# Optimization experiments

Measured on AMD Instinct MI355X. Metric: run time of the kernel, lower is better.

Reference implementation:

```python
import jax, jax.numpy as jnp
import numpy as np

B, S, D = 1, 2048, 2048
H, G, HD = 32, 8, 64          # heads, kv groups, head_dim
GS = H // G                   # group size = 4
EPS = 1e-6


def _rmsnorm(v, w):
    vf = v.astype(jnp.float32)
    n = vf * jax.lax.rsqrt(jnp.mean(vf * vf, axis=-1, keepdims=True) + EPS)
    return (n * (1.0 + w.astype(jnp.float32))).astype(v.dtype)


def _rope(v, cos, sin):
    # v: [b, h, s, hd]; cos/sin: [s, hd] (rot_dim == head_dim)
    half = v.shape[-1] // 2
    x1, x2 = v[..., :half], v[..., half:]
    rotated = jnp.concatenate([-x2, x1], axis=-1)
    c = cos[None, None, :, :]
    s = sin[None, None, :, :]
    return (v * c + rotated * s).astype(v.dtype)


def setup_inputs() -> dict:
    key = jax.random.key(0)
    ks = jax.random.split(key, 8)
    x = jax.random.normal(ks[0], (B, S, D), dtype=jnp.float32)
    # causal mask: True above diagonal => masked out
    mask = jnp.triu(jnp.ones((S, S), dtype=bool), k=1)
    # standard RoPE tables, full rotary dim == head_dim
    inv_freq = 1.0 / (10000.0 ** (jnp.arange(0, HD, 2, dtype=jnp.float32) / HD))
    angles = jnp.arange(S, dtype=jnp.float32)[:, None] * inv_freq[None, :]
    angles = jnp.concatenate([angles, angles], axis=-1)  # [S, HD]
    cos = jnp.cos(angles)
    sin = jnp.sin(angles)
    sc = 1.0 / np.sqrt(D)
    Wq = jax.random.normal(ks[1], (2 * H * HD, D), dtype=jnp.float32) * sc
    Wk = jax.random.normal(ks[2], (G * HD, D), dtype=jnp.float32) * sc
    Wv = jax.random.normal(ks[3], (G * HD, D), dtype=jnp.float32) * sc
    Wo = jax.random.normal(ks[4], (D, H * HD), dtype=jnp.float32) * sc
    q_norm_w = jnp.zeros((HD,), dtype=jnp.float32)
    k_norm_w = jnp.zeros((HD,), dtype=jnp.float32)
    return {"x": x, "mask": mask, "cos": cos, "sin": sin, "Wq": Wq,
            "Wk": Wk, "Wv": Wv, "Wo": Wo,
            "q_norm_w": q_norm_w, "k_norm_w": k_norm_w}


def reference(x, mask, cos, sin, Wq, Wk, Wv, Wo, q_norm_w, k_norm_w):
    b, s, _ = x.shape
    d_out = H * HD
    # fused q + gate projection: [b, s, H, 2*HD]
    qg = jnp.einsum('bsd,ed->bse', x, Wq).reshape(b, s, H, 2 * HD)
    q = qg[..., :HD]                         # [b, s, H, HD]
    gate = qg[..., HD:].reshape(b, s, d_out)  # [b, s, d_out]
    k = jnp.einsum('bsd,ed->bse', x, Wk).reshape(b, s, G, HD)
    v = jnp.einsum('bsd,ed->bse', x, Wv).reshape(b, s, G, HD)
    q = q.transpose(0, 2, 1, 3)   # [b, H, s, HD]
    k = k.transpose(0, 2, 1, 3)   # [b, G, s, HD]
    v = v.transpose(0, 2, 1, 3)
    q = _rmsnorm(q, q_norm_w)
    k = _rmsnorm(k, k_norm_w)
    q = _rope(q, cos[:s], sin[:s])
    k = _rope(k, cos[:s], sin[:s])
    # GQA without materializing repeated K/V: group queries as [b, G, GS, s, HD]
    qg_ = q.reshape(b, G, GS, s, HD)
    scores = jnp.einsum('bghqd,bgkd->bghqk', qg_, k)   # [b, G, GS, s, s]
    scores = jnp.where(mask[None, None, None, :s, :s], -jnp.inf, scores)
    scale = HD ** (-0.5)
    w = jax.nn.softmax((scores * scale).astype(jnp.float32), axis=-1).astype(q.dtype)
    ctx = jnp.einsum('bghqk,bgkd->bghqd', w, v)        # [b, G, GS, s, HD]
    ctx = ctx.reshape(b, H, s, HD).transpose(0, 2, 1, 3).reshape(b, s, d_out)
    ctx = ctx * jax.nn.sigmoid(gate)
    return jnp.einsum('bse,de->bsd', ctx, Wo)
```

## Files before the change

### kernel.cpp

```cpp
#include <hip/hip_runtime.h>

typedef __bf16 bf16;
typedef __bf16 bf16x4 __attribute__((ext_vector_type(4)));
typedef __bf16 bf16x8 __attribute__((ext_vector_type(8)));
typedef float f32x4 __attribute__((ext_vector_type(4)));

#define DEV static __device__ __forceinline__

constexpr int S  = 2048;
constexpr int D  = 2048;
constexpr int H  = 32;
constexpr int G  = 8;
constexpr int HD = 64;
constexpr int NQG = 2 * H * HD;
constexpr int LDP = 136;

DEV bf16x8 load8(const bf16* p) { return *reinterpret_cast<const bf16x8*>(p); }

DEV f32x4 mfma16(bf16x8 a, bf16x8 b, f32x4 c) {
  return __builtin_amdgcn_mfma_f32_16x16x32_bf16(a, b, c, 0, 0, 0);
}

DEV void gload_lds16(const bf16* g, bf16* l) {
  __builtin_amdgcn_global_load_lds(
      (const __attribute__((address_space(1))) void*)g,
      (__attribute__((address_space(3))) void*)l, 16, 0, 0);
}

#define BARRIER() asm volatile("s_barrier" ::: "memory")
#define VMDRAIN() asm volatile("s_waitcnt vmcnt(0)" ::: "memory")

template <int NISS>
DEV void stage_tile(bf16* lds, const bf16* src_row0, size_t ld, int k0, int tid) {
  const int w = tid >> 6, l = tid & 63;
#pragma unroll
  for (int i = 0; i < NISS; ++i) {
    int blk = w * NISS + i;
    int r = blk * 8 + (l >> 3);
    int c = (l & 7) ^ (r & 7);
    gload_lds16(src_row0 + (size_t)r * ld + k0 + c * 8, lds + blk * 512);
  }
}

DEV void stage64_8w(bf16* lds, const bf16* src_row0, size_t ld, int k0, int tid) {
  const int w = tid >> 6, l = tid & 63;
  int r = w * 8 + (l >> 3);
  int c = (l & 7) ^ (r & 7);
  gload_lds16(src_row0 + (size_t)r * ld + k0 + c * 8, lds + w * 512);
}

DEV bf16x8 fragr(const bf16* T, int row, int chunk) {
  return load8(T + row * 64 + (((chunk ^ (row & 7)) << 3)));
}

DEV float fexp2(float x) { return __builtin_amdgcn_exp2f(x); }
DEV float frcp(float x)  { return __builtin_amdgcn_rcpf(x); }

__global__ __launch_bounds__(256) void cvt_all(
    const float* __restrict__ x,  const float* __restrict__ wq,
    const float* __restrict__ wk, const float* __restrict__ wv,
    bf16* __restrict__ xb,  bf16* __restrict__ wqb, bf16* __restrict__ wkb,
    bf16* __restrict__ wvb)
{
  long c = (long)blockIdx.x * 256 + threadIdx.x;
  const float* src; bf16* dst; long off;
  if      (c <  524288) { src = x;  dst = xb;  off = c; }
  else if (c < 1572864) { src = wq; dst = wqb; off = c -  524288; }
  else if (c < 1703936) { src = wk; dst = wkb; off = c - 1572864; }
  else                  { src = wv; dst = wvb; off = c - 1703936; }
  long i = off * 8;
  const float4* p = reinterpret_cast<const float4*>(src + i);
  float4 a = p[0], b = p[1];
  bf16x8 o;
  o[0] = (bf16)a.x; o[1] = (bf16)a.y; o[2] = (bf16)a.z; o[3] = (bf16)a.w;
  o[4] = (bf16)b.x; o[5] = (bf16)b.y; o[6] = (bf16)b.z; o[7] = (bf16)b.w;
  *reinterpret_cast<bf16x8*>(dst + i) = o;
}

DEV void rms_rope_store(f32x4 acc[4][4], bf16* __restrict__ dst,
                        const float* __restrict__ w,
                        const float* __restrict__ cosb,
                        const float* __restrict__ sinb,
                        int s0, int ln, int hi, float outscale)
{
  float wgt[4];
#pragma unroll
  for (int ni = 0; ni < 4; ++ni) wgt[ni] = 1.0f + w[ni * 16 + ln];
#pragma unroll
  for (int mi = 0; mi < 4; ++mi)
#pragma unroll
    for (int j = 0; j < 4; ++j) {
      int s = s0 + mi * 16 + hi * 4 + j;
      float v0 = acc[mi][0][j], v1 = acc[mi][1][j];
      float v2 = acc[mi][2][j], v3 = acc[mi][3][j];
      float ss = v0 * v0 + v1 * v1 + v2 * v2 + v3 * v3;
      ss += __shfl_xor(ss, 1);
      ss += __shfl_xor(ss, 2);
      ss += __shfl_xor(ss, 4);
      ss += __shfl_xor(ss, 8);
      float inv = __builtin_amdgcn_rsqf(ss * (1.0f / 64.0f) + 1e-6f);
      float xf[4] = {v0 * inv * wgt[0], v1 * inv * wgt[1],
                     v2 * inv * wgt[2], v3 * inv * wgt[3]};
#pragma unroll
      for (int ni = 0; ni < 4; ++ni) {
        int d = ni * 16 + ln;
        float c  = cosb[s * HD + d];
        float sn = sinb[s * HD + d];
        float rot = (ni < 2) ? -xf[ni + 2] : xf[ni - 2];
        dst[(size_t)s * HD + d] = (bf16)((xf[ni] * c + rot * sn) * outscale);
      }
    }
}

__global__ __launch_bounds__(256, 3) void gemm_qkv(
    const bf16* __restrict__ X, const bf16* __restrict__ Wq,
    const bf16* __restrict__ Wk, const bf16* __restrict__ Wv,
    const float* __restrict__ cosb, const float* __restrict__ sinb,
    const float* __restrict__ qw, const float* __restrict__ kw,
    const float* __restrict__ wo, bf16* __restrict__ wob,
    bf16* __restrict__ qg, bf16* __restrict__ qrot,
    bf16* __restrict__ krot, bf16* __restrict__ vt)
{
  __shared__ __align__(16) bf16 As[128 * 64];
  __shared__ __align__(16) bf16 Bs[128 * 64];

  const int tid  = threadIdx.x;
  const int nt = blockIdx.x;

  if (nt >= 40) {
    long base = (long)((nt - 40) * 16 + blockIdx.y) * 256 + tid;
#pragma unroll
    for (int it = 0; it < 16; ++it) {
      long i = (base + (long)it * 32768) * 8;
      const float4* p = reinterpret_cast<const float4*>(wo + i);
      float4 a = p[0], b = p[1];
      bf16x8 o;
      o[0] = (bf16)a.x; o[1] = (bf16)a.y; o[2] = (bf16)a.z; o[3] = (bf16)a.w;
      o[4] = (bf16)b.x; o[5] = (bf16)b.y; o[6] = (bf16)b.z; o[7] = (bf16)b.w;
      *reinterpret_cast<bf16x8*>(wob + i) = o;
    }
    return;
  }

  const int wave = tid >> 6;
  const int lane = tid & 63;
  const int ln = lane & 15, hi = lane >> 4;
  const int wm = wave >> 1, wn = wave & 1;
  const int m0 = blockIdx.y * 128;

  const bf16* W; int n0;
  if (nt < 32)      { W = Wq; n0 = nt * 128; }
  else if (nt < 36) { W = Wk; n0 = (nt - 32) * 128; }
  else              { W = Wv; n0 = (nt - 36) * 128; }

  const bf16* arow = X + (size_t)m0 * D;
  const bf16* brow = W + (size_t)n0 * D;

  f32x4 acc[4][4] = {};

  for (int k0 = 0; k0 < D; k0 += 64) {
    __syncthreads();
    stage_tile<4>(As, arow, D, k0, tid);
    stage_tile<4>(Bs, brow, D, k0, tid);
    __syncthreads();
#pragma unroll
    for (int kk = 0; kk < 64; kk += 32) {
      bf16x8 a[4], b[4];
#pragma unroll
      for (int mi = 0; mi < 4; ++mi) a[mi] = fragr(As, wm * 64 + mi * 16 + ln, (kk >> 3) + hi);
#pragma unroll
      for (int ni = 0; ni < 4; ++ni) b[ni] = fragr(Bs, wn * 64 + ni * 16 + ln, (kk >> 3) + hi);
#pragma unroll
      for (int mi = 0; mi < 4; ++mi)
#pragma unroll
        for (int ni = 0; ni < 4; ++ni)
          acc[mi][ni] = mfma16(a[mi], b[ni], acc[mi][ni]);
    }
  }

  const int s0 = m0 + wm * 64;
  if (nt < 32) {
    if (wn == 0) {
      rms_rope_store(acc, qrot + (size_t)nt * S * HD, qw, cosb, sinb,
                     s0, ln, hi, 0.18033688011111204f);
    } else {
#pragma unroll
      for (int mi = 0; mi < 4; ++mi)
#pragma unroll
        for (int ni = 0; ni < 4; ++ni)
#pragma unroll
          for (int j = 0; j < 4; ++j) {
            int r = s0 + mi * 16 + hi * 4 + j;
            int c = nt * 128 + 64 + ni * 16 + ln;
            qg[(size_t)r * NQG + c] = (bf16)acc[mi][ni][j];
          }
    }
  } else if (nt < 36) {
    int g8 = (nt - 32) * 2 + wn;
    rms_rope_store(acc, krot + (size_t)g8 * S * HD, kw, cosb, sinb,
                   s0, ln, hi, 1.0f);
  } else {
    int nrel = (nt - 36) * 128;
#pragma unroll
    for (int mi = 0; mi < 4; ++mi)
#pragma unroll
      for (int ni = 0; ni < 4; ++ni)
#pragma unroll
        for (int j = 0; j < 4; ++j) {
          int r = s0 + mi * 16 + hi * 4 + j;
          int c = nrel + wn * 64 + ni * 16 + ln;
          vt[(size_t)c * S + r] = (bf16)acc[mi][ni][j];
        }
  }
}

__global__ __launch_bounds__(256, 3) void gemm_out(
    const bf16* __restrict__ A, const bf16* __restrict__ W,
    float* __restrict__ C)
{
  __shared__ __align__(16) bf16 As[128 * 64];
  __shared__ __align__(16) bf16 Bs[64 * 64];

  const int tid  = threadIdx.x;
  const int wave = tid >> 6;
  const int lane = tid & 63;
  const int ln = lane & 15, hi = lane >> 4;
  const int m0 = blockIdx.y * 128;
  const int n0 = blockIdx.x * 64;

  const bf16* arow = A + (size_t)m0 * D;
  const bf16* brow = W + (size_t)n0 * D;

  f32x4 acc[2][4] = {};

  for (int k0 = 0; k0 < D; k0 += 64) {
    __syncthreads();
    stage_tile<4>(As, arow, D, k0, tid);
    stage_tile<2>(Bs, brow, D, k0, tid);
    __syncthreads();
#pragma unroll
    for (int kk = 0; kk < 64; kk += 32) {
      bf16x8 a[2], b[4];
#pragma unroll
      for (int mi = 0; mi < 2; ++mi) a[mi] = fragr(As, wave * 32 + mi * 16 + ln, (kk >> 3) + hi);
#pragma unroll
      for (int ni = 0; ni < 4; ++ni) b[ni] = fragr(Bs, ni * 16 + ln, (kk >> 3) + hi);
#pragma unroll
      for (int mi = 0; mi < 2; ++mi)
#pragma unroll
        for (int ni = 0; ni < 4; ++ni)
          acc[mi][ni] = mfma16(a[mi], b[ni], acc[mi][ni]);
    }
  }

#pragma unroll
  for (int mi = 0; mi < 2; ++mi)
#pragma unroll
    for (int ni = 0; ni < 4; ++ni)
#pragma unroll
      for (int j = 0; j < 4; ++j) {
        int r = m0 + wave * 32 + mi * 16 + hi * 4 + j;
        int c = n0 + ni * 16 + ln;
        C[(size_t)r * D + c] = acc[mi][ni][j];
      }
}

DEV void attn_phase(const bf16* __restrict__ qrot, const bf16* __restrict__ krow,
                    const bf16* __restrict__ vrow, const bf16* __restrict__ qg,
                    bf16* __restrict__ ctxg,
                    bf16* Kbase, bf16* Vbase, bf16* pw,
                    int h, int qchunk, int ln, int hi, int tid)
{
  const int nt = (qchunk >> 1) + 1;
  const int qb = qchunk * 64 + ((tid >> 6) & 3) * 16;
  const int q  = qb + ln;

  const bf16* qbase = qrot + ((size_t)h * S + qb + ln) * HD + hi * 8;
  bf16x8 q0 = load8(qbase);
  bf16x8 q1 = load8(qbase + 32);

  f32x4 po[4] = {};
  float m = -INFINITY, l = 0.f;

  stage64_8w(Kbase,        krow,            64, 0,  tid);
  stage64_8w(Kbase + 4096, krow + 64 * 64,  64, 0,  tid);
  stage64_8w(Vbase,        vrow,            S,  0,  tid);
  stage64_8w(Vbase + 4096, vrow,            S,  64, tid);
  VMDRAIN();
  BARRIER();

  int cur = 0;
  for (int t = 0; t < nt; ++t) {
    const bf16* Kc = Kbase + cur * 8192;
    const bf16* Vc = Vbase + cur * 8192;

    if (t + 1 < nt) {
      bf16* Kn = Kbase + (cur ^ 1) * 8192;
      bf16* Vn = Vbase + (cur ^ 1) * 8192;
      stage64_8w(Kn,        krow + (size_t)(t + 1) * 128 * 64,        64, 0, tid);
      stage64_8w(Kn + 4096, krow + ((size_t)(t + 1) * 128 + 64) * 64, 64, 0, tid);
      stage64_8w(Vn,        vrow, S, (t + 1) * 128,      tid);
      stage64_8w(Vn + 4096, vrow, S, (t + 1) * 128 + 64, tid);
    }

    f32x4 sc[2][4];
#pragma unroll
    for (int s = 0; s < 2; ++s) {
      const bf16* Ks = Kc + s * 4096;
      bf16x8 kf0[4], kf1[4];
#pragma unroll
      for (int kr = 0; kr < 4; ++kr) {
        kf0[kr] = fragr(Ks, kr * 16 + ln, hi);
        kf1[kr] = fragr(Ks, kr * 16 + ln, hi + 4);
      }
      __builtin_amdgcn_s_setprio(1);
#pragma unroll
      for (int kr = 0; kr < 4; ++kr) {
        f32x4 z = {};
        z = mfma16(kf0[kr], q0, z);
        sc[s][kr] = mfma16(kf1[kr], q1, z);
      }
      __builtin_amdgcn_s_setprio(0);
    }

    float pmax = -INFINITY;
    if (t == nt - 1) {
      const int key0 = t * 128;
#pragma unroll
      for (int s = 0; s < 2; ++s)
#pragma unroll
        for (int kr = 0; kr < 4; ++kr)
#pragma unroll
          for (int j = 0; j < 4; ++j) {
            int key = key0 + s * 64 + kr * 16 + hi * 4 + j;
            float v = (key <= q) ? sc[s][kr][j] : -INFINITY;
            sc[s][kr][j] = v;
            pmax = fmaxf(pmax, v);
          }
    } else {
#pragma unroll
      for (int s = 0; s < 2; ++s)
#pragma unroll
        for (int kr = 0; kr < 4; ++kr)
#pragma unroll
          for (int j = 0; j < 4; ++j) pmax = fmaxf(pmax, sc[s][kr][j]);
    }
    pmax = fmaxf(pmax, __shfl_xor(pmax, 16));
    pmax = fmaxf(pmax, __shfl_xor(pmax, 32));

    if (__any(pmax > m + 8.0f)) {
      float mn = fmaxf(m, pmax);
      float c  = fexp2(m - mn);
      l *= c;
      float cc[4];
#pragma unroll
      for (int j = 0; j < 4; ++j) cc[j] = __shfl(c, hi * 4 + j);
#pragma unroll
      for (int dt = 0; dt < 4; ++dt)
#pragma unroll
        for (int j = 0; j < 4; ++j) po[dt][j] *= cc[j];
      m = mn;
    }

    float ps = 0.f;
#pragma unroll
    for (int s = 0; s < 2; ++s)
#pragma unroll
      for (int kr = 0; kr < 4; ++kr)
#pragma unroll
        for (int j = 0; j < 4; ++j) {
          float e = fexp2(sc[s][kr][j] - m);
          sc[s][kr][j] = e;
          ps += e;
        }
    ps += __shfl_xor(ps, 16);
    ps += __shfl_xor(ps, 32);
    l += ps;

#pragma unroll
    for (int s = 0; s < 2; ++s)
#pragma unroll
      for (int kr = 0; kr < 4; ++kr) {
        unsigned w0, w1;
        asm("v_cvt_pk_bf16_f32 %0, %1, %2" : "=v"(w0) : "v"(sc[s][kr][0]), "v"(sc[s][kr][1]));
        asm("v_cvt_pk_bf16_f32 %0, %1, %2" : "=v"(w1) : "v"(sc[s][kr][2]), "v"(sc[s][kr][3]));
        uint2 w = {w0, w1};
        *reinterpret_cast<uint2*>(pw + ln * LDP + s * 64 + kr * 16 + hi * 4) = w;
      }
    bf16x8 pa[4];
#pragma unroll
    for (int sl = 0; sl < 4; ++sl) pa[sl] = load8(pw + ln * LDP + sl * 32 + hi * 8);

    __builtin_amdgcn_s_setprio(1);
#pragma unroll
    for (int sl = 0; sl < 4; ++sl) {
      const bf16* Vs = Vc + (sl >> 1) * 4096;
      const int ch = (sl & 1) * 4 + hi;
#pragma unroll
      for (int dt = 0; dt < 4; ++dt)
        po[dt] = mfma16(pa[sl], fragr(Vs, dt * 16 + ln, ch), po[dt]);
    }
    __builtin_amdgcn_s_setprio(0);

    VMDRAIN();
    BARRIER();
    cur ^= 1;
  }

  float lf[4];
#pragma unroll
  for (int j = 0; j < 4; ++j) lf[j] = __shfl(l, hi * 4 + j);
#pragma unroll
  for (int dt = 0; dt < 4; ++dt)
#pragma unroll
    for (int j = 0; j < 4; ++j) {
      int qq = qb + hi * 4 + j;
      int d  = dt * 16 + ln;
      float o  = po[dt][j] * frcp(lf[j]);
      float gv = (float)qg[(size_t)qq * NQG + h * 128 + 64 + d];
      float sg = frcp(1.0f + fexp2(gv * -1.442695040888963f));
      ctxg[(size_t)qq * D + h * 64 + d] = (bf16)(o * sg);
    }
}

__global__ __launch_bounds__(512) void attn(
    const bf16* __restrict__ qrot, const bf16* __restrict__ krot,
    const bf16* __restrict__ vt, const bf16* __restrict__ qg,
    bf16* __restrict__ ctxg)
{
  __shared__ __align__(16) bf16 Kbuf[2][2][64 * 64];
  __shared__ __align__(16) bf16 Vbuf[2][2][64 * 64];
  __shared__ __align__(16) bf16 Pl[8][16 * LDP];

  const int tid  = threadIdx.x;
  const int lane = tid & 63;
  const int ln = lane & 15, hi = lane >> 4;

  const int bid = blockIdx.x;
  const int g   = bid & 7;
  const int i   = bid >> 3;
  const int hp  = i & 1;
  const int pr  = i >> 1;
  const int h   = g * 4 + hp * 2 + ((tid >> 6) >> 2);
  bf16* pw = &Pl[tid >> 6][0];

  const bf16* krow = krot + (size_t)g * S * HD;
  const bf16* vrow = vt + (size_t)g * 64 * S;

  attn_phase(qrot, krow, vrow, qg, ctxg,
             &Kbuf[0][0][0], &Vbuf[0][0][0], pw, h, pr, ln, hi, tid);
  attn_phase(qrot, krow, vrow, qg, ctxg,
             &Kbuf[0][0][0], &Vbuf[0][0][0], pw, h, 31 - pr, ln, hi, tid);
}

extern "C" void kernel_launch(void* const* d_in, const int* in_sizes, int n_in,
                              void* d_out, int out_size, void* d_ws, size_t ws_size,
                              hipStream_t stream) {
  const float* x    = (const float*)d_in[0];
  const float* cosb = (const float*)d_in[2];
  const float* sinb = (const float*)d_in[3];
  const float* Wq   = (const float*)d_in[4];
  const float* Wk   = (const float*)d_in[5];
  const float* Wv   = (const float*)d_in[6];
  const float* Wo   = (const float*)d_in[7];
  const float* qw   = (const float*)d_in[8];
  const float* kw   = (const float*)d_in[9];

  char* ws = (char*)d_ws;
  bf16* xb   = (bf16*)(ws);
  bf16* Wqb  = (bf16*)(ws + ( 8u << 20));
  bf16* Wkb  = (bf16*)(ws + (24u << 20));
  bf16* Wvb  = (bf16*)(ws + (26u << 20));
  bf16* Wob  = (bf16*)(ws + (28u << 20));
  bf16* qg   = (bf16*)(ws + (36u << 20));
  bf16* vt   = (bf16*)(ws + (54u << 20));
  bf16* qrot = (bf16*)(ws + (56u << 20));
  bf16* krot = (bf16*)(ws + (64u << 20));
  bf16* ctxg = (bf16*)(ws + (66u << 20));
  float* out = (float*)d_out;

  cvt_all<<<dim3(7168), 256, 0, stream>>>(x, Wq, Wk, Wv, xb, Wqb, Wkb, Wvb);

  gemm_qkv<<<dim3(48, 16), 256, 0, stream>>>(xb, Wqb, Wkb, Wvb,
                                             cosb, sinb, qw, kw,
                                             Wo, Wob,
                                             qg, qrot, krot, vt);
  attn<<<dim3(256), 512, 0, stream>>>(qrot, krot, vt, qg, ctxg);
  gemm_out<<<dim3(32, 16), 256, 0, stream>>>(ctxg, Wob, out);
}
```

Measured before the change: 130.6 us.

## Double-buffer LDS prefetch in QKV and output GEMMs, enlarge out-proj tile

Both GEMM kernels now keep two LDS stages and issue async global-to-LDS loads two k-tiles ahead, waiting with a partial vmcnt so that loads overlap MFMA work. MFMA sections are wrapped with raised wave priority. The output projection moves to 128x128 tiles with a 2x2 wave layout, halving the block count. The larger LDS footprint lowers occupancy to two blocks per CU, and gemm_out now launches only one block per CU.

```diff
diff --git a/kernel.cpp b/kernel.cpp
--- a/kernel.cpp
+++ b/kernel.cpp
@@ -27,8 +27,9 @@
       (__attribute__((address_space(3))) void*)l, 16, 0, 0);
 }
 
-#define BARRIER() asm volatile("s_barrier" ::: "memory")
-#define VMDRAIN() asm volatile("s_waitcnt vmcnt(0)" ::: "memory")
+#define BARRIER()  asm volatile("s_barrier" ::: "memory")
+#define VMDRAIN()  asm volatile("s_waitcnt vmcnt(0)" ::: "memory")
+#define VMWAIT8()  asm volatile("s_waitcnt vmcnt(8)" ::: "memory")
 
 template <int NISS>
 DEV void stage_tile(bf16* lds, const bf16* src_row0, size_t ld, int k0, int tid) {
@@ -112,7 +113,7 @@
     }
 }
 
-__global__ __launch_bounds__(256, 3) void gemm_qkv(
+__global__ __launch_bounds__(256, 2) void gemm_qkv(
     const bf16* __restrict__ X, const bf16* __restrict__ Wq,
     const bf16* __restrict__ Wk, const bf16* __restrict__ Wv,
     const float* __restrict__ cosb, const float* __restrict__ sinb,
@@ -121,11 +122,11 @@
     bf16* __restrict__ qg, bf16* __restrict__ qrot,
     bf16* __restrict__ krot, bf16* __restrict__ vt)
 {
-  __shared__ __align__(16) bf16 As[128 * 64];
-  __shared__ __align__(16) bf16 Bs[128 * 64];
-
-  const int tid  = threadIdx.x;
-  const int nt = blockIdx.x;
+  __shared__ __align__(16) bf16 As[2][128 * 64];
+  __shared__ __align__(16) bf16 Bs[2][128 * 64];
+
+  const int tid = threadIdx.x;
+  const int nt  = blockIdx.x;
 
   if (nt >= 40) {
     long base = (long)((nt - 40) * 16 + blockIdx.y) * 256 + tid;
@@ -158,24 +159,41 @@
 
   f32x4 acc[4][4] = {};
 
-  for (int k0 = 0; k0 < D; k0 += 64) {
-    __syncthreads();
-    stage_tile<4>(As, arow, D, k0, tid);
-    stage_tile<4>(Bs, brow, D, k0, tid);
-    __syncthreads();
+  stage_tile<4>(As[0], arow, D, 0, tid);
+  stage_tile<4>(Bs[0], brow, D, 0, tid);
+  stage_tile<4>(As[1], arow, D, 64, tid);
+  stage_tile<4>(Bs[1], brow, D, 64, tid);
+  VMWAIT8();
+  BARRIER();
+
+  constexpr int NT = D / 64;
+  for (int t = 0; t < NT; ++t) {
+    const bf16* Asc = As[t & 1];
+    const bf16* Bsc = Bs[t & 1];
 #pragma unroll
     for (int kk = 0; kk < 64; kk += 32) {
       bf16x8 a[4], b[4];
 #pragma unroll
-      for (int mi = 0; mi < 4; ++mi) a[mi] = fragr(As, wm * 64 + mi * 16 + ln, (kk >> 3) + hi);
-#pragma unroll
-      for (int ni = 0; ni < 4; ++ni) b[ni] = fragr(Bs, wn * 64 + ni * 16 + ln, (kk >> 3) + hi);
+      for (int mi = 0; mi < 4; ++mi) a[mi] = fragr(Asc, wm * 64 + mi * 16 + ln, (kk >> 3) + hi);
+#pragma unroll
+      for (int ni = 0; ni < 4; ++ni) b[ni] = fragr(Bsc, wn * 64 + ni * 16 + ln, (kk >> 3) + hi);
+      __builtin_amdgcn_s_setprio(1);
 #pragma unroll
       for (int mi = 0; mi < 4; ++mi)
 #pragma unroll
         for (int ni = 0; ni < 4; ++ni)
           acc[mi][ni] = mfma16(a[mi], b[ni], acc[mi][ni]);
-    }
+      __builtin_amdgcn_s_setprio(0);
+    }
+    BARRIER();
+    if (t + 2 < NT) {
+      stage_tile<4>(As[t & 1], arow, D, (t + 2) * 64, tid);
+      stage_tile<4>(Bs[t & 1], brow, D, (t + 2) * 64, tid);
+      VMWAIT8();
+    } else if (t + 1 < NT) {
+      VMDRAIN();
+    }
+    BARRIER();
   }
 
   const int s0 = m0 + wm * 64;
@@ -214,53 +232,71 @@
   }
 }
 
-__global__ __launch_bounds__(256, 3) void gemm_out(
+__global__ __launch_bounds__(256, 2) void gemm_out(
     const bf16* __restrict__ A, const bf16* __restrict__ W,
     float* __restrict__ C)
 {
-  __shared__ __align__(16) bf16 As[128 * 64];
-  __shared__ __align__(16) bf16 Bs[64 * 64];
+  __shared__ __align__(16) bf16 As[2][128 * 64];
+  __shared__ __align__(16) bf16 Bs[2][128 * 64];
 
   const int tid  = threadIdx.x;
   const int wave = tid >> 6;
   const int lane = tid & 63;
   const int ln = lane & 15, hi = lane >> 4;
+  const int wm = wave >> 1, wn = wave & 1;
   const int m0 = blockIdx.y * 128;
-  const int n0 = blockIdx.x * 64;
+  const int n0 = blockIdx.x * 128;
 
   const bf16* arow = A + (size_t)m0 * D;
   const bf16* brow = W + (size_t)n0 * D;
 
-  f32x4 acc[2][4] = {};
-
-  for (int k0 = 0; k0 < D; k0 += 64) {
-    __syncthreads();
-    stage_tile<4>(As, arow, D, k0, tid);
-    stage_tile<2>(Bs, brow, D, k0, tid);
-    __syncthreads();
+  f32x4 acc[4][4] = {};
+
+  stage_tile<4>(As[0], arow, D, 0, tid);
+  stage_tile<4>(Bs[0], brow, D, 0, tid);
+  stage_tile<4>(As[1], arow, D, 64, tid);
+  stage_tile<4>(Bs[1], brow, D, 64, tid);
+  VMWAIT8();
+  BARRIER();
+
+  constexpr int NT = D / 64;
+  for (int t = 0; t < NT; ++t) {
+    const bf16* Asc = As[t & 1];
+    const bf16* Bsc = Bs[t & 1];
 #pragma unroll
     for (int kk = 0; kk < 64; kk += 32) {
-      bf16x8 a[2], b[4];
-#pragma unroll
-      for (int mi = 0; mi < 2; ++mi) a[mi] = fragr(As, wave * 32 + mi * 16 + ln, (kk >> 3) + hi);
-#pragma unroll
-      for (int ni = 0; ni < 4; ++ni) b[ni] = fragr(Bs, ni * 16 + ln, (kk >> 3) + hi);
-#pragma unroll
-      for (int mi = 0; mi < 2; ++mi)
+      bf16x8 a[4], b[4];
+#pragma unroll
+      for (int mi = 0; mi < 4; ++mi) a[mi] = fragr(Asc, wm * 64 + mi * 16 + ln, (kk >> 3) + hi);
+#pragma unroll
+      for (int ni = 0; ni < 4; ++ni) b[ni] = fragr(Bsc, wn * 64 + ni * 16 + ln, (kk >> 3) + hi);
+      __builtin_amdgcn_s_setprio(1);
+#pragma unroll
+      for (int mi = 0; mi < 4; ++mi)
 #pragma unroll
         for (int ni = 0; ni < 4; ++ni)
           acc[mi][ni] = mfma16(a[mi], b[ni], acc[mi][ni]);
-    }
+      __builtin_amdgcn_s_setprio(0);
+    }
+    BARRIER();
+    if (t + 2 < NT) {
+      stage_tile<4>(As[t & 1], arow, D, (t + 2) * 64, tid);
+      stage_tile<4>(Bs[t & 1], brow, D, (t + 2) * 64, tid);
+      VMWAIT8();
+    } else if (t + 1 < NT) {
+      VMDRAIN();
+    }
+    BARRIER();
   }
 
 #pragma unroll
-  for (int mi = 0; mi < 2; ++mi)
+  for (int mi = 0; mi < 4; ++mi)
 #pragma unroll
     for (int ni = 0; ni < 4; ++ni)
 #pragma unroll
       for (int j = 0; j < 4; ++j) {
-        int r = m0 + wave * 32 + mi * 16 + hi * 4 + j;
-        int c = n0 + ni * 16 + ln;
+        int r = m0 + wm * 64 + mi * 16 + hi * 4 + j;
+        int c = n0 + wn * 64 + ni * 16 + ln;
         C[(size_t)r * D + c] = acc[mi][ni][j];
       }
 }
@@ -486,5 +522,5 @@
                                              Wo, Wob,
                                              qg, qrot, krot, vt);
   attn<<<dim3(256), 512, 0, stream>>>(qrot, krot, vt, qg, ctxg);
-  gemm_out<<<dim3(32, 16), 256, 0, stream>>>(ctxg, Wob, out);
-}
+  gemm_out<<<dim3(16, 16), 256, 0, stream>>>(ctxg, Wob, out);
+}
```

Result: slower. 157.7 us (+20.7%).
